# Kernel optimization log

Measured on AMD Instinct MI355X. Metric: run time of the kernel, lower is better.

Reference implementation:

```python
import jax, jax.numpy as jnp
import numpy as np

HD = 1960            # 40 channels * 49 kernel taps
KH = KW = 7
PH = PW = 3
SH = SW = 3


def _patch_idx(out_len, k, s):
    return (jnp.arange(out_len) * s)[:, None] + jnp.arange(k)[None, :]  # [out_len, k]


def _unfold(img, kh, kw, ph, pw, sh, sw):
    # img: [N, C, Hi, Wi] -> cols: [N, C*kh*kw, Hout*Wout]  (torch F.unfold layout)
    N, C, Hi, Wi = img.shape
    Hout = (Hi + 2 * ph - kh) // sh + 1
    Wout = (Wi + 2 * pw - kw) // sw + 1
    xp = jnp.pad(img, ((0, 0), (0, 0), (ph, ph), (pw, pw)))
    ii = _patch_idx(Hout, kh, sh)  # [Hout, kh]
    jj = _patch_idx(Wout, kw, sw)  # [Wout, kw]
    p = xp[:, :, ii[:, :, None, None], jj[None, None, :, :]]  # [N,C,Hout,kh,Wout,kw]
    p = p.transpose(0, 1, 3, 5, 2, 4).reshape(N, C * kh * kw, Hout * Wout)
    return p


def _fold(cols, out_h, out_w, kh, kw, ph, pw, sh, sw):
    # cols: [N, C*kh*kw, L] -> img: [N, C, out_h, out_w]  (torch F.fold overlap-add)
    N, CK, L = cols.shape
    C = CK // (kh * kw)
    Hout = (out_h + 2 * ph - kh) // sh + 1
    Wout = (out_w + 2 * pw - kw) // sw + 1
    p = cols.reshape(N, C, kh, kw, Hout, Wout).transpose(0, 1, 4, 2, 5, 3)  # [N,C,Hout,kh,Wout,kw]
    ii = _patch_idx(Hout, kh, sh)
    jj = _patch_idx(Wout, kw, sw)
    out = jnp.zeros((N, C, out_h + 2 * ph, out_w + 2 * pw), cols.dtype)
    out = out.at[:, :, ii[:, :, None, None], jj[None, None, :, :]].add(p)
    return out[:, :, ph:out_h + ph, pw:out_w + pw]


def _dwconv(x, w, b, pad):
    # depthwise conv, x: [N,C,H,W], w: [C,1,k,k]
    y = jax.lax.conv_general_dilated(
        x, w, window_strides=(1, 1), padding=[(pad, pad), (pad, pad)],
        dimension_numbers=('NCHW', 'OIHW', 'NCHW'), feature_group_count=x.shape[1])
    return y + b[None, :, None, None]


def setup_inputs() -> dict:
    key = jax.random.key(0)
    ks = jax.random.split(key, 6)
    d_model = 512
    x = jax.random.normal(ks[0], (2, 5760, d_model), dtype=jnp.float32)
    w1 = jax.random.normal(ks[1], (d_model, HD), dtype=jnp.float32) * 0.02
    b1 = jnp.zeros((HD,), jnp.float32)
    w3 = jax.random.normal(ks[2], (HD // 2, 1, 3, 3), dtype=jnp.float32) * 0.1
    b3 = jnp.zeros((HD // 2,), jnp.float32)
    w5 = jax.random.normal(ks[3], (HD - HD // 2, 1, 5, 5), dtype=jnp.float32) * 0.05
    b5 = jnp.zeros((HD - HD // 2,), jnp.float32)
    w2 = jax.random.normal(ks[4], (HD, d_model), dtype=jnp.float32) * 0.02
    b2 = jnp.zeros((d_model,), jnp.float32)
    return dict(x=x, w1=w1, b1=b1, w3=w3, b3=b3, w5=w5, b5=b5, w2=w2, b2=b2,
                out_h=60, out_w=108, T=8, H=20, W=36)


def reference(x, w1, b1, w3, b3, w5, b5, w2, b2, out_h, out_w, T, H, W):
    n_vecs = ((out_h + 2 * PH - KH) // SH + 1) * ((out_w + 2 * PW - KW) // SW + 1)
    x = x @ w1 + b1                                   # [b, n, hd]
    b, n, c = x.shape
    cols = x.reshape(-1, n_vecs, c).transpose(0, 2, 1)  # [b*T, hd, n_vecs]
    bt = cols.shape[0]
    img = _fold(cols, out_h, out_w, KH, KW, PH, PW, SH, SW)           # [b*T, 40, out_h, out_w]
    norm = _fold(jnp.ones((bt, KH * KW, n_vecs), x.dtype),
                 out_h, out_w, KH, KW, PH, PW, SH, SW)                # [b*T, 1, out_h, out_w]
    cols2 = _unfold(img / norm, KH, KW, PH, PW, SH, SW)               # [b*T, hd, n_vecs]
    x = cols2.transpose(0, 2, 1).reshape(b, n, c)
    x = x.reshape(b * T, H, W, c).transpose(0, 3, 1, 2)               # [b*T, hd, H, W]
    h = c // 2
    y = jnp.concatenate([_dwconv(x[:, :h], w3, b3, 1),
                         _dwconv(x[:, h:], w5, b5, 2)], axis=1)       # MixConv2d (depthwise 3x3 / 5x5)
    y = y.transpose(0, 2, 3, 1).reshape(b, n, c)
    return jax.nn.gelu(y, approximate=False) @ w2 + b2
```

## Files before the change

### kernel.cpp

```cpp
#include <hip/hip_runtime.h>
#include <cstdint>

typedef short v8s __attribute__((ext_vector_type(8)));
typedef float v4f __attribute__((ext_vector_type(4)));
typedef unsigned short u16;

#define M_ROWS 11520
#define K1 512
#define N1 2048
#define C_REAL 1960
#define K2 1984
#define N2 512
#define TPAD 56
#define PLANE_ELEMS (720 * TPAD)
#define HROW 2016

__device__ __forceinline__ u16 f2b(float f) {
  union { float f; unsigned u; } v; v.f = f;
  unsigned r = v.u + 0x7FFFu + ((v.u >> 16) & 1u);
  return (u16)(r >> 16);
}
__device__ __forceinline__ float b2f(u16 b) {
  union { unsigned u; float f; } v; v.u = ((unsigned)b) << 16; return v.f;
}

__device__ __forceinline__ void gl2lds16(const u16* g, u16* l) {
  __builtin_amdgcn_global_load_lds(
      (const __attribute__((address_space(1))) unsigned int*)g,
      (__attribute__((address_space(3))) unsigned int*)l, 16, 0, 0);
}

__global__ void cast_x8(const float* __restrict__ x, u16* __restrict__ xb) {
  int i = blockIdx.x * 256 + threadIdx.x;
  const float4 a = ((const float4*)x)[2 * i];
  const float4 b = ((const float4*)x)[2 * i + 1];
  u16 o[8] = {f2b(a.x), f2b(a.y), f2b(a.z), f2b(a.w),
              f2b(b.x), f2b(b.y), f2b(b.z), f2b(b.w)};
  ((int4*)xb)[i] = *(const int4*)o;
}

__global__ __launch_bounds__(256) void transpose_cast(
    const float* __restrict__ src, u16* __restrict__ dst, int R, int C, int KP)
{
  __shared__ float T[32][33];
  const int n0 = blockIdx.x * 32, k0 = blockIdx.y * 32;
  const int tx = threadIdx.x & 31, ty = threadIdx.x >> 5;
  #pragma unroll
  for (int r = 0; r < 4; ++r) {
    int k = k0 + ty + 8 * r, n = n0 + tx;
    T[ty + 8 * r][tx] = (k < R && n < C) ? src[(size_t)k * C + n] : 0.f;
  }
  __syncthreads();
  #pragma unroll
  for (int r = 0; r < 4; ++r) {
    int n = n0 + ty + 8 * r, k = k0 + tx;
    if (k < KP) dst[(size_t)n * KP + k] = f2b(T[tx][ty + 8 * r]);
  }
}

__global__ void zero_gpad(u16* __restrict__ G) {
  int i = blockIdx.x * 256 + threadIdx.x;
  int r = i / 24, j = i - r * 24;
  G[(size_t)r * K2 + C_REAL + j] = 0;
}

__device__ __forceinline__ void stv(float v, float* p) { *p = v; }
__device__ __forceinline__ void stv(float v, u16* p) { *p = f2b(v); }

template<typename OT, bool FOLD>
__global__ __launch_bounds__(256) void gemm_bt(
    const u16* __restrict__ A, const u16* __restrict__ BT,
    const float* __restrict__ bias, int nb, OT* __restrict__ C, int N, int K)
{
  __shared__ u16 As[128 * 64];
  __shared__ u16 Bs[128 * 64];
  const int tid = threadIdx.x;
  const int bm = blockIdx.y * 128, bn = blockIdx.x * 128;
  const int wave = tid >> 6, lane = tid & 63;
  const int quad = lane >> 4, l16 = lane & 15;
  const int wm = (wave >> 1) * 64, wn = (wave & 1) * 64;
  const int srow = lane >> 3;
  const int scol = ((lane & 7) ^ srow) * 8;

  const u16* pA = A + (size_t)(bm + wave * 32 + srow) * K + scol;
  const u16* pB = BT + (size_t)(bn + wave * 32 + srow) * K + scol;
  u16* lA = As + (wave * 32) * 64;
  u16* lB = Bs + (wave * 32) * 64;

  v4f acc[4][4];
  #pragma unroll
  for (int i = 0; i < 4; ++i)
    #pragma unroll
    for (int j = 0; j < 4; ++j) acc[i][j] = (v4f){0.f, 0.f, 0.f, 0.f};

  for (int k0 = 0; k0 < K; k0 += 64) {
    #pragma unroll
    for (int q = 0; q < 4; ++q) {
      gl2lds16(pA + (size_t)(q * 8) * K, lA + q * 8 * 64);
      gl2lds16(pB + (size_t)(q * 8) * K, lB + q * 8 * 64);
    }
    pA += 64; pB += 64;
    __syncthreads();
    #pragma unroll
    for (int h = 0; h < 2; ++h) {
      v8s af[4], bf[4];
      #pragma unroll
      for (int i = 0; i < 4; ++i) {
        int row = wm + i * 16 + l16;
        int ck = (h * 4 + quad) ^ (row & 7);
        af[i] = *(const v8s*)&As[row * 64 + ck * 8];
      }
      #pragma unroll
      for (int j = 0; j < 4; ++j) {
        int row = wn + j * 16 + l16;
        int ck = (h * 4 + quad) ^ (row & 7);
        bf[j] = *(const v8s*)&Bs[row * 64 + ck * 8];
      }
      #pragma unroll
      for (int i = 0; i < 4; ++i)
        #pragma unroll
        for (int j = 0; j < 4; ++j)
          acc[i][j] = __builtin_amdgcn_mfma_f32_16x16x32_bf16(af[i], bf[j], acc[i][j], 0, 0, 0);
    }
    __syncthreads();
  }

  #pragma unroll
  for (int i = 0; i < 4; ++i) {
    #pragma unroll
    for (int j = 0; j < 4; ++j) {
      int col = bn + wn + j * 16 + l16;
      if (FOLD && col >= C_REAL) continue;
      float bv = (col < nb) ? bias[col] : 0.f;
      int ch = 0, t = 0;
      if (FOLD) { ch = col / 49; t = col - ch * 49; }
      #pragma unroll
      for (int r = 0; r < 4; ++r) {
        int row = bm + wm + i * 16 + quad * 4 + r;
        float val = acc[i][j][r] + bv;
        if (FOLD) {
          int bt = row / 720, v = row - bt * 720;
          stv(val, C + (size_t)(bt * 40 + ch) * PLANE_ELEMS + v * TPAD + t);
        } else {
          stv(val, C + (size_t)row * N + col);
        }
      }
    }
  }
}

__global__ __launch_bounds__(256) void fold_norm(const u16* __restrict__ Aw,
                                                 float* __restrict__ Sn)
{
  __shared__ u16 raw[10 * HROW];
  const int plane = blockIdx.y;
  const int r0 = blockIdx.x * 22;
  const int tid = threadIdx.x;
  const int hlo = max(0, (r0 - 6) / 3);
  const int hhi = min(19, (r0 + 21) / 3);
  const int nchunks = (hhi - hlo + 1) * (HROW / 8);
  const int4* src = (const int4*)(Aw + (size_t)plane * PLANE_ELEMS + hlo * HROW);
  int4* dst = (int4*)raw;
  for (int j = tid; j < nchunks; j += 256) dst[j] = src[j];
  __syncthreads();

  float* out = Sn + (size_t)plane * 7524 + r0 * 114;
  for (int i = tid; i < 22 * 114; i += 256) {
    int r = i / 114, px = i - r * 114;
    int py = r0 + r;
    float val = 0.f;
    if (py >= 3 && py < 63 && px >= 3 && px < 111) {
      int ry = py % 3, rx = px % 3;
      int hhs[3], kis[3], nki = 0;
      #pragma unroll
      for (int k = 0; k < 3; ++k) {
        int ki = ry + 3 * k;
        if (ki < 7 && py - ki >= 0) {
          int hh = (py - ki) / 3;
          if (hh < 20) { kis[nki] = ki; hhs[nki] = hh; ++nki; }
        }
      }
      int wws[3], kjs[3], nkj = 0;
      #pragma unroll
      for (int k = 0; k < 3; ++k) {
        int kj = rx + 3 * k;
        if (kj < 7 && px - kj >= 0) {
          int ww = (px - kj) / 3;
          if (ww < 36) { kjs[nkj] = kj; wws[nkj] = ww; ++nkj; }
        }
      }
      float sum = 0.f;
      for (int a = 0; a < nki; ++a) {
        int rowoff = (hhs[a] - hlo) * HROW + kis[a] * 7;
        for (int b = 0; b < nkj; ++b)
          sum += b2f(raw[rowoff + wws[b] * TPAD + kjs[b]]);
      }
      val = sum / (float)(nki * nkj);
    }
    out[i] = val;
  }
}

template<int KS>
__device__ __forceinline__ void conv_col(const float* __restrict__ Sl,
    const float* __restrict__ Wl, const float* __restrict__ Bl,
    u16* __restrict__ G, int bt, int colbase, int tid)
{
  constexpr int P = KS / 2;
  for (int idx = tid; idx < 36 * 49; idx += 512) {
    int wo = idx / 49, t = idx - wo * 49;
    int ki = t / 7, kj = t - ki * 7;
    float wgt[KS * KS];
    #pragma unroll
    for (int j = 0; j < KS * KS; ++j) wgt[j] = Wl[t * KS * KS + j];
    const float bias = Bl[t];
    int sx[KS]; bool vx[KS];
    #pragma unroll
    for (int dx = 0; dx < KS; ++dx) {
      int wq = wo + dx - P;
      vx[dx] = (wq >= 0 && wq < 36);
      sx[dx] = wq * 3 + kj;
    }
    float win[KS][KS];
    #pragma unroll
    for (int dy = 0; dy < KS; ++dy) {
      int hq = dy - P;
      #pragma unroll
      for (int dx = 0; dx < KS; ++dx)
        win[dy][dx] = (hq >= 0 && vx[dx]) ? Sl[(hq * 3 + ki) * 114 + sx[dx]] : 0.f;
    }
    u16* gp = G + (size_t)(bt * 720 + wo) * K2 + colbase + t;
    for (int h = 0; h < 20; ++h) {
      float y = bias;
      #pragma unroll
      for (int dy = 0; dy < KS; ++dy)
        #pragma unroll
        for (int dx = 0; dx < KS; ++dx)
          y += wgt[dy * KS + dx] * win[dy][dx];
      float g = 0.5f * y * (1.0f + erff(y * 0.70710678118654752f));
      *gp = f2b(g);
      gp += (size_t)36 * K2;
      if (h < 19) {
        #pragma unroll
        for (int dy = 0; dy < KS - 1; ++dy)
          #pragma unroll
          for (int dx = 0; dx < KS; ++dx) win[dy][dx] = win[dy + 1][dx];
        int hq = h + 1 + P;
        #pragma unroll
        for (int dx = 0; dx < KS; ++dx)
          win[KS - 1][dx] = (hq < 20 && vx[dx])
                              ? Sl[(hq * 3 + ki) * 114 + sx[dx]] : 0.f;
      }
    }
  }
}

__global__ __launch_bounds__(512) void dwconv_gelu3(const float* __restrict__ Sn,
    const float* __restrict__ w3, const float* __restrict__ b3,
    const float* __restrict__ w5, const float* __restrict__ b5,
    u16* __restrict__ G)
{
  __shared__ float Sl[66 * 114];
  __shared__ float Wl[49 * 25];
  __shared__ float Bl[49];
  const int plane = blockIdx.x, bt = plane / 40, ch = plane % 40;
  const int tid = threadIdx.x;
  const int colbase = ch * 49;
  const bool is3 = (ch < 20);
  if (is3) {
    for (int i = tid; i < 49 * 9; i += 512) Wl[i] = w3[colbase * 9 + i];
    if (tid < 49) Bl[tid] = b3[colbase + tid];
  } else {
    int c5 = colbase - 980;
    for (int i = tid; i < 49 * 25; i += 512) Wl[i] = w5[c5 * 25 + i];
    if (tid < 49) Bl[tid] = b5[c5 + tid];
  }
  const float4* sp = (const float4*)(Sn + (size_t)plane * 7524);
  float4* sl4 = (float4*)Sl;
  for (int i = tid; i < 7524 / 4; i += 512) sl4[i] = sp[i];
  __syncthreads();
  if (is3) conv_col<3>(Sl, Wl, Bl, G, bt, colbase, tid);
  else     conv_col<5>(Sl, Wl, Bl, G, bt, colbase, tid);
}

extern "C" void kernel_launch(void* const* d_in, const int* in_sizes, int n_in,
                              void* d_out, int out_size, void* d_ws, size_t ws_size,
                              hipStream_t stream) {
  const float* x  = (const float*)d_in[0];
  const float* w1 = (const float*)d_in[1];
  const float* b1 = (const float*)d_in[2];
  const float* w3 = (const float*)d_in[3];
  const float* b3 = (const float*)d_in[4];
  const float* w5 = (const float*)d_in[5];
  const float* b5 = (const float*)d_in[6];
  const float* w2 = (const float*)d_in[7];
  const float* b2 = (const float*)d_in[8];
  float* out = (float*)d_out;

  char* ws = (char*)d_ws;
  u16*   Xb  = (u16*)(ws);
  u16*   W1T = (u16*)(ws + 11796480);
  u16*   W2T = (u16*)(ws + 13893632);
  u16*   Aw  = (u16*)(ws + 15925248);
  u16*   G   = (u16*)(ws + 67534848);
  float* Sn  = (float*)(ws + 113246208);

  hipLaunchKernelGGL(cast_x8, dim3(2880), dim3(256), 0, stream, x, Xb);
  hipLaunchKernelGGL(transpose_cast, dim3(64, 16), dim3(256), 0, stream, w1, W1T, K1, C_REAL, K1);
  hipLaunchKernelGGL(transpose_cast, dim3(16, 62), dim3(256), 0, stream, w2, W2T, C_REAL, N2, K2);
  hipLaunchKernelGGL(zero_gpad, dim3(1080), dim3(256), 0, stream, G);
  hipLaunchKernelGGL((gemm_bt<u16, true>), dim3(N1 / 128, M_ROWS / 128), dim3(256), 0, stream,
                     Xb, W1T, b1, C_REAL, Aw, N1, K1);
  hipLaunchKernelGGL(fold_norm, dim3(3, 640), dim3(256), 0, stream, Aw, Sn);
  hipLaunchKernelGGL(dwconv_gelu3, dim3(640), dim3(512), 0, stream,
                     Sn, w3, b3, w5, b5, G);
  hipLaunchKernelGGL((gemm_bt<float, false>), dim3(N2 / 128, M_ROWS / 128), dim3(256), 0, stream,
                     G, W2T, b2, N2, out, N2, K2);
}
```

Measured before the change: 272.4 us.

## Merge prep kernels into one launch and enlarge first GEMM tile to 256 rows

```diff
diff --git a/kernel.cpp b/kernel.cpp
--- a/kernel.cpp
+++ b/kernel.cpp
@@ -30,21 +30,40 @@
       (__attribute__((address_space(3))) unsigned int*)l, 16, 0, 0);
 }
 
-__global__ void cast_x8(const float* __restrict__ x, u16* __restrict__ xb) {
-  int i = blockIdx.x * 256 + threadIdx.x;
-  const float4 a = ((const float4*)x)[2 * i];
-  const float4 b = ((const float4*)x)[2 * i + 1];
-  u16 o[8] = {f2b(a.x), f2b(a.y), f2b(a.z), f2b(a.w),
-              f2b(b.x), f2b(b.y), f2b(b.z), f2b(b.w)};
-  ((int4*)xb)[i] = *(const int4*)o;
-}
-
-__global__ __launch_bounds__(256) void transpose_cast(
-    const float* __restrict__ src, u16* __restrict__ dst, int R, int C, int KP)
+__global__ __launch_bounds__(256) void prep(
+    const float* __restrict__ x,  u16* __restrict__ xb,
+    const float* __restrict__ w1, u16* __restrict__ W1T,
+    const float* __restrict__ w2, u16* __restrict__ W2T,
+    u16* __restrict__ G)
 {
   __shared__ float T[32][33];
-  const int n0 = blockIdx.x * 32, k0 = blockIdx.y * 32;
-  const int tx = threadIdx.x & 31, ty = threadIdx.x >> 5;
+  int b = blockIdx.x;
+  const int tid = threadIdx.x;
+  if (b < 2880) {
+    int i = b * 256 + tid;
+    const float4 a = ((const float4*)x)[2 * i];
+    const float4 c = ((const float4*)x)[2 * i + 1];
+    u16 o[8] = {f2b(a.x), f2b(a.y), f2b(a.z), f2b(a.w),
+                f2b(c.x), f2b(c.y), f2b(c.z), f2b(c.w)};
+    ((int4*)xb)[i] = *(const int4*)o;
+    return;
+  }
+  b -= 2880;
+  const float* src; u16* dst; int R, C, KP, n0, k0;
+  if (b < 1024) {
+    src = w1; dst = W1T; R = K1; C = C_REAL; KP = K1;
+    n0 = (b & 63) * 32; k0 = (b >> 6) * 32;
+  } else if (b < 2016) {
+    int bb = b - 1024;
+    src = w2; dst = W2T; R = C_REAL; C = N2; KP = K2;
+    n0 = (bb & 15) * 32; k0 = (bb >> 4) * 32;
+  } else {
+    int i = (b - 2016) * 256 + tid;
+    int r = i / 24, j = i - r * 24;
+    G[(size_t)r * K2 + C_REAL + j] = 0;
+    return;
+  }
+  const int tx = tid & 31, ty = tid >> 5;
   #pragma unroll
   for (int r = 0; r < 4; ++r) {
     int k = k0 + ty + 8 * r, n = n0 + tx;
@@ -58,22 +77,93 @@
   }
 }
 
-__global__ void zero_gpad(u16* __restrict__ G) {
-  int i = blockIdx.x * 256 + threadIdx.x;
-  int r = i / 24, j = i - r * 24;
-  G[(size_t)r * K2 + C_REAL + j] = 0;
-}
-
 __device__ __forceinline__ void stv(float v, float* p) { *p = v; }
 __device__ __forceinline__ void stv(float v, u16* p) { *p = f2b(v); }
 
-template<typename OT, bool FOLD>
-__global__ __launch_bounds__(256) void gemm_bt(
+__global__ __launch_bounds__(512) void gemm1_fold(
     const u16* __restrict__ A, const u16* __restrict__ BT,
-    const float* __restrict__ bias, int nb, OT* __restrict__ C, int N, int K)
+    const float* __restrict__ bias, u16* __restrict__ C)
+{
+  __shared__ u16 As[256 * 64];
+  __shared__ u16 Bs[128 * 64];
+  const int K = K1, N = N1;
+  const int tid = threadIdx.x;
+  const int bm = blockIdx.y * 256, bn = blockIdx.x * 128;
+  const int wave = tid >> 6, lane = tid & 63;
+  const int quad = lane >> 4, l16 = lane & 15;
+  const int wm = (wave >> 1) * 64, wn = (wave & 1) * 64;
+  const int srow = lane >> 3;
+  const int scol = ((lane & 7) ^ srow) * 8;
+
+  const u16* pA = A + (size_t)(bm + wave * 32 + srow) * K + scol;
+  const u16* pB = BT + (size_t)(bn + wave * 16 + srow) * K + scol;
+  u16* lA = As + (wave * 32) * 64;
+  u16* lB = Bs + (wave * 16) * 64;
+
+  v4f acc[4][4];
+  #pragma unroll
+  for (int i = 0; i < 4; ++i)
+    #pragma unroll
+    for (int j = 0; j < 4; ++j) acc[i][j] = (v4f){0.f, 0.f, 0.f, 0.f};
+
+  for (int k0 = 0; k0 < K; k0 += 64) {
+    #pragma unroll
+    for (int q = 0; q < 4; ++q)
+      gl2lds16(pA + (size_t)(q * 8) * K, lA + q * 8 * 64);
+    #pragma unroll
+    for (int q = 0; q < 2; ++q)
+      gl2lds16(pB + (size_t)(q * 8) * K, lB + q * 8 * 64);
+    pA += 64; pB += 64;
+    __syncthreads();
+    #pragma unroll
+    for (int h = 0; h < 2; ++h) {
+      v8s af[4], bf[4];
+      #pragma unroll
+      for (int i = 0; i < 4; ++i) {
+        int row = wm + i * 16 + l16;
+        int ck = (h * 4 + quad) ^ (row & 7);
+        af[i] = *(const v8s*)&As[row * 64 + ck * 8];
+      }
+      #pragma unroll
+      for (int j = 0; j < 4; ++j) {
+        int row = wn + j * 16 + l16;
+        int ck = (h * 4 + quad) ^ (row & 7);
+        bf[j] = *(const v8s*)&Bs[row * 64 + ck * 8];
+      }
+      #pragma unroll
+      for (int i = 0; i < 4; ++i)
+        #pragma unroll
+        for (int j = 0; j < 4; ++j)
+          acc[i][j] = __builtin_amdgcn_mfma_f32_16x16x32_bf16(af[i], bf[j], acc[i][j], 0, 0, 0);
+    }
+    __syncthreads();
+  }
+
+  #pragma unroll
+  for (int i = 0; i < 4; ++i) {
+    #pragma unroll
+    for (int j = 0; j < 4; ++j) {
+      int col = bn + wn + j * 16 + l16;
+      if (col >= C_REAL) continue;
+      float bv = bias[col];
+      int ch = col / 49, t = col - ch * 49;
+      #pragma unroll
+      for (int r = 0; r < 4; ++r) {
+        int row = bm + wm + i * 16 + quad * 4 + r;
+        int bt = row / 720, v = row - bt * 720;
+        C[(size_t)(bt * 40 + ch) * PLANE_ELEMS + v * TPAD + t] = f2b(acc[i][j][r] + bv);
+      }
+    }
+  }
+}
+
+__global__ __launch_bounds__(256) void gemm2(
+    const u16* __restrict__ A, const u16* __restrict__ BT,
+    const float* __restrict__ bias, float* __restrict__ C)
 {
   __shared__ u16 As[128 * 64];
   __shared__ u16 Bs[128 * 64];
+  const int K = K2, N = N2;
   const int tid = threadIdx.x;
   const int bm = blockIdx.y * 128, bn = blockIdx.x * 128;
   const int wave = tid >> 6, lane = tid & 63;
@@ -130,20 +220,11 @@
     #pragma unroll
     for (int j = 0; j < 4; ++j) {
       int col = bn + wn + j * 16 + l16;
-      if (FOLD && col >= C_REAL) continue;
-      float bv = (col < nb) ? bias[col] : 0.f;
-      int ch = 0, t = 0;
-      if (FOLD) { ch = col / 49; t = col - ch * 49; }
+      float bv = bias[col];
       #pragma unroll
       for (int r = 0; r < 4; ++r) {
         int row = bm + wm + i * 16 + quad * 4 + r;
-        float val = acc[i][j][r] + bv;
-        if (FOLD) {
-          int bt = row / 720, v = row - bt * 720;
-          stv(val, C + (size_t)(bt * 40 + ch) * PLANE_ELEMS + v * TPAD + t);
-        } else {
-          stv(val, C + (size_t)row * N + col);
-        }
+        C[(size_t)row * N + col] = acc[i][j][r] + bv;
       }
     }
   }
@@ -305,15 +386,13 @@
   u16*   G   = (u16*)(ws + 67534848);
   float* Sn  = (float*)(ws + 113246208);
 
-  hipLaunchKernelGGL(cast_x8, dim3(2880), dim3(256), 0, stream, x, Xb);
-  hipLaunchKernelGGL(transpose_cast, dim3(64, 16), dim3(256), 0, stream, w1, W1T, K1, C_REAL, K1);
-  hipLaunchKernelGGL(transpose_cast, dim3(16, 62), dim3(256), 0, stream, w2, W2T, C_REAL, N2, K2);
-  hipLaunchKernelGGL(zero_gpad, dim3(1080), dim3(256), 0, stream, G);
-  hipLaunchKernelGGL((gemm_bt<u16, true>), dim3(N1 / 128, M_ROWS / 128), dim3(256), 0, stream,
-                     Xb, W1T, b1, C_REAL, Aw, N1, K1);
+  hipLaunchKernelGGL(prep, dim3(5976), dim3(256), 0, stream,
+                     x, Xb, w1, W1T, w2, W2T, G);
+  hipLaunchKernelGGL(gemm1_fold, dim3(N1 / 128, M_ROWS / 256), dim3(512), 0, stream,
+                     Xb, W1T, b1, Aw);
   hipLaunchKernelGGL(fold_norm, dim3(3, 640), dim3(256), 0, stream, Aw, Sn);
   hipLaunchKernelGGL(dwconv_gelu3, dim3(640), dim3(512), 0, stream,
                      Sn, w3, b3, w5, b5, G);
-  hipLaunchKernelGGL((gemm_bt<float, false>), dim3(N2 / 128, M_ROWS / 128), dim3(256), 0, stream,
-                     G, W2T, b2, N2, out, N2, K2);
-}
+  hipLaunchKernelGGL(gemm2, dim3(N2 / 128, M_ROWS / 128), dim3(256), 0, stream,
+                     G, W2T, b2, out);
+}
```

New measurement: 259.0 us. 1.05x faster.
